# Performance work log

Hardware: AMD Instinct MI355X
Metric: run time of the kernel (lower is better)

Reference implementation:

```python
import jax, jax.numpy as jnp
import numpy as np

NUM_HEADS = 12
DIM = 768
HEAD_DIM = DIM // NUM_HEADS
SCALE = HEAD_DIM ** -0.5
LORA_ALPHA = 1.0


def setup_inputs() -> dict:
    key = jax.random.key(0)
    ks = jax.random.split(key, 9)
    B, H, W = 1, 64, 64
    return {
        "x": jax.random.normal(ks[0], (B, H, W, DIM), jnp.float32),
        "w_qkv": jax.random.normal(ks[1], (3 * DIM, DIM), jnp.float32) * 0.02,
        "b_qkv": jax.random.normal(ks[2], (3 * DIM,), jnp.float32) * 0.02,
        "lora_A": jax.random.normal(ks[3], (12, DIM), jnp.float32) * 0.02,
        "lora_B": jax.random.normal(ks[4], (3 * DIM, 12), jnp.float32) * 0.02,
        "w_proj": jax.random.normal(ks[5], (DIM, DIM), jnp.float32) * 0.02,
        "b_proj": jax.random.normal(ks[6], (DIM,), jnp.float32) * 0.02,
        "rel_pos_h": jax.random.normal(ks[7], (2 * H - 1, HEAD_DIM), jnp.float32) * 0.02,
        "rel_pos_w": jax.random.normal(ks[8], (2 * W - 1, HEAD_DIM), jnp.float32) * 0.02,
    }


def _get_rel_pos(size: int, rel_pos: jnp.ndarray) -> jnp.ndarray:
    # q_size == k_size and rel_pos.shape[0] == 2*size-1, so no interpolation.
    coords = jnp.arange(size)[:, None] - jnp.arange(size)[None, :] + (size - 1)
    return rel_pos[coords]  # [size, size, head_dim]


def reference(x, w_qkv, b_qkv, lora_A, lora_B, w_proj, b_proj, rel_pos_h, rel_pos_w):
    B, H, W, _ = x.shape
    N = H * W
    # LoRA qkv projection: W_eff path = base + alpha * x @ (B A)^T
    qkv = x @ w_qkv.T + b_qkv + LORA_ALPHA * ((x @ lora_A.T) @ lora_B.T)
    qkv = qkv.reshape(B, N, 3, NUM_HEADS, HEAD_DIM)
    qkv = jnp.transpose(qkv, (2, 0, 3, 1, 4)).reshape(3, B * NUM_HEADS, N, HEAD_DIM)
    q, k, v = qkv[0], qkv[1], qkv[2]
    attn = jnp.einsum('bqc,bkc->bqk', q * SCALE, k)  # [B*nh, N, N]
    # decomposed relative position bias
    Rh = _get_rel_pos(H, rel_pos_h)  # [H, H, hd]
    Rw = _get_rel_pos(W, rel_pos_w)  # [W, W, hd]
    r_q = q.reshape(B * NUM_HEADS, H, W, HEAD_DIM)
    rel_h = jnp.einsum('bhwc,hkc->bhwk', r_q, Rh)
    rel_w = jnp.einsum('bhwc,wkc->bhwk', r_q, Rw)
    attn = (attn.reshape(-1, H, W, H, W)
            + rel_h[:, :, :, :, None]
            + rel_w[:, :, :, None, :]).reshape(-1, N, N)
    attn = jax.nn.softmax(attn, axis=-1)
    out = jnp.einsum('bqk,bkc->bqc', attn, v)  # [B*nh, N, hd]
    out = out.reshape(B, NUM_HEADS, H, W, HEAD_DIM)
    out = jnp.transpose(out, (0, 2, 3, 1, 4)).reshape(B, H, W, DIM)
    return out @ w_proj.T + b_proj
```

## Files before the change

### kernel.cpp

```cpp
#include <hip/hip_runtime.h>
#include <stdint.h>


typedef __attribute__((ext_vector_type(4))) float f32x4;
typedef __attribute__((ext_vector_type(16))) float f32x16;
typedef __attribute__((ext_vector_type(4))) float fvec4;
typedef __attribute__((ext_vector_type(8))) short s16x8;
typedef __attribute__((ext_vector_type(4))) short s16x4;
typedef __attribute__((ext_vector_type(4))) unsigned u32x4;

constexpr int NH  = 12;
constexpr int HD  = 64;
constexpr int DIM = 768;
constexpr int N   = 4096;
constexpr int QKV = 2304;
constexpr float LOG2E  = 1.4426950408889634f;
constexpr float SCALE2 = 0.125f * LOG2E;

static __device__ __forceinline__ short f2bf(float f) {
  unsigned u = __builtin_bit_cast(unsigned, f);
  unsigned r = (u + 0x7FFFu + ((u >> 16) & 1u)) >> 16;
  return (short)r;
}
static __device__ __forceinline__ float bf2f(short s) {
  unsigned u = ((unsigned)(unsigned short)s) << 16;
  return __builtin_bit_cast(float, u);
}
static __device__ __forceinline__ unsigned cvt_pk_bf16(float a, float b) {
  unsigned r;
  asm("v_cvt_pk_bf16_f32 %0, %1, %2" : "=v"(r) : "v"(a), "v"(b));
  return r;
}
static __device__ __forceinline__ float ex2(float x) {
  float r;
  asm("v_exp_f32 %0, %1" : "=v"(r) : "v"(x));
  return r;
}
static __device__ __forceinline__ void gload16(const void* g, void* l) {
  __builtin_amdgcn_global_load_lds(
      (const __attribute__((address_space(1))) void*)g,
      (__attribute__((address_space(3))) void*)l, 16, 0, 0);
}

__global__ __launch_bounds__(256) void k_weff(const float* __restrict__ w_qkv,
                                              const float* __restrict__ lora_A,
                                              const float* __restrict__ lora_B,
                                              short* __restrict__ weff) {
  int e = blockIdx.x * 256 + threadIdx.x;
  if (e >= QKV * DIM) return;
  int r = e / DIM, c = e % DIM;
  float acc = w_qkv[e];
#pragma unroll
  for (int t = 0; t < 12; ++t) acc += lora_B[r * 12 + t] * lora_A[t * DIM + c];
  weff[e] = f2bf(acc);
}

__global__ __launch_bounds__(256) void k_x2bf(const float* __restrict__ x,
                                              short* __restrict__ xb) {
  int i = blockIdx.x * 256 + threadIdx.x;
  fvec4 v = *reinterpret_cast<const fvec4*>(x + (size_t)i * 4);
  s16x4 p;
  p[0] = f2bf(v[0]); p[1] = f2bf(v[1]); p[2] = f2bf(v[2]); p[3] = f2bf(v[3]);
  *reinterpret_cast<s16x4*>(xb + (size_t)i * 4) = p;
}

__global__ __launch_bounds__(256) void k_wsplit(const float* __restrict__ w,
                                                short* __restrict__ ws) {
  int r = blockIdx.y;
  int kk = blockIdx.x * 256 + threadIdx.x;
  int blk = (kk >= 1536) ? 2 : (kk >= 768 ? 1 : 0);
  int c = kk - blk * 768;
  float wv = w[(size_t)r * 768 + c];
  short hi = f2bf(wv);
  ws[(size_t)r * 2304 + kk] = (blk == 1) ? f2bf(wv - bf2f(hi)) : hi;
}

template <int KIT, int MODE, int BM>
__global__ __launch_bounds__(256) void k_gemm(const short* __restrict__ A,
                                              const short* __restrict__ B,
                                              const float* __restrict__ bias,
                                              short* __restrict__ qo,
                                              short* __restrict__ ko,
                                              short* __restrict__ vo,
                                              float* __restrict__ outf) {
  constexpr int MFR = BM / 32;
  __shared__ __align__(16) char lds[BM * 128 + 16384];
  const int tid = threadIdx.x;
  const int wave = tid >> 6, lane = tid & 63, lr = lane & 15, lg = lane >> 4;
  const int wr = wave >> 1, wc = wave & 1;
  const int i0 = blockIdx.x * BM, j0 = blockIdx.y * 128;
  const int LDA = KIT * 128;

  size_t offA[MFR], offB[4];
#pragma unroll
  for (int it = 0; it < MFR; ++it) {
    int c = it * 256 + tid;
    int row = c >> 3;
    offA[it] = (size_t)row * LDA + (((c & 7) << 4) ^ ((row & 7) << 4));
  }
#pragma unroll
  for (int it = 0; it < 4; ++it) {
    int c = it * 256 + tid;
    int row = c >> 3;
    offB[it] = (size_t)row * LDA + (((c & 7) << 4) ^ ((row & 7) << 4));
  }
  const char* Ab = (const char*)A + (size_t)i0 * LDA;
  const char* Bb = (const char*)B + (size_t)j0 * LDA;
  char* la = lds + wave * 1024;
  char* lb = lds + BM * 128 + wave * 1024;

  const int swz = (lr & 7) << 4;
  const int ab = (wr * (BM / 2) + lr) * 128 + ((lg * 16) ^ swz);
  const int bb = BM * 128 + (wc * 64 + lr) * 128 + ((lg * 16) ^ swz);

  f32x4 acc[MFR][4] = {};

  for (int kt = 0; kt < KIT; ++kt) {
    const size_t kadd = (size_t)kt * 128;
#pragma unroll
    for (int it = 0; it < MFR; ++it) gload16(Ab + kadd + offA[it], la + it * 4096);
#pragma unroll
    for (int it = 0; it < 4; ++it) gload16(Bb + kadd + offB[it], lb + it * 4096);
    __syncthreads();
#pragma unroll
    for (int ks2 = 0; ks2 < 2; ++ks2) {
      s16x8 af[MFR], bf_[4];
#pragma unroll
      for (int m = 0; m < MFR; ++m)
        af[m] = *reinterpret_cast<const s16x8*>(lds + ((ab + m * 2048) ^ (ks2 << 6)));
#pragma unroll
      for (int n = 0; n < 4; ++n)
        bf_[n] = *reinterpret_cast<const s16x8*>(lds + ((bb + n * 2048) ^ (ks2 << 6)));
#pragma unroll
      for (int m = 0; m < MFR; ++m)
#pragma unroll
        for (int n = 0; n < 4; ++n)
          acc[m][n] = __builtin_amdgcn_mfma_f32_16x16x32_bf16(af[m], bf_[n], acc[m][n], 0, 0, 0);
    }
    __syncthreads();
  }

  if constexpr (MODE == 0) {
    const int three = j0 / 768;
    const int head = ((j0 % 768) >> 6) + wc;
    short* dst = (three == 0) ? qo : ((three == 1) ? ko : vo);
#pragma unroll
    for (int n = 0; n < 4; ++n) {
      const int col = n * 16 + lr;
      const float bj = bias[j0 + wc * 64 + col];
#pragma unroll
      for (int m = 0; m < MFR; ++m)
#pragma unroll
        for (int r = 0; r < 4; ++r) {
          int i = i0 + wr * (BM / 2) + m * 16 + lg * 4 + r;
          dst[((size_t)head * N + i) * HD + col] = f2bf(acc[m][n][r] + bj);
        }
    }
  } else {
#pragma unroll
    for (int n = 0; n < 4; ++n) {
      const int j = j0 + wc * 64 + n * 16 + lr;
      const float bj = bias[j];
#pragma unroll
      for (int m = 0; m < MFR; ++m)
#pragma unroll
        for (int r = 0; r < 4; ++r) {
          int i = i0 + wr * (BM / 2) + m * 16 + lg * 4 + r;
          outf[(size_t)i * 768 + j] = acc[m][n][r] + bj;
        }
    }
  }
}

__global__ __launch_bounds__(256) void k_vT(const short* __restrict__ vg,
                                            short* __restrict__ vTg) {
  __shared__ short ts[64 * 72];
  const int tid = threadIdx.x;
  const int i0 = blockIdx.x * 64;
  const int h = blockIdx.y;
#pragma unroll
  for (int it = 0; it < 2; ++it) {
    int ch = tid + 256 * it;
    int row = ch >> 3, cc = (ch & 7) * 8;
    *reinterpret_cast<s16x8*>(&ts[row * 72 + cc]) =
        *reinterpret_cast<const s16x8*>(&vg[((size_t)h * N + i0 + row) * HD + cc]);
  }
  __syncthreads();
#pragma unroll
  for (int it = 0; it < 2; ++it) {
    int ch = tid + 256 * it;
    int c = ch >> 3, ii = (ch & 7) * 8;
    s16x8 o;
#pragma unroll
    for (int j = 0; j < 8; ++j) o[j] = ts[(ii + j) * 72 + c];
    *reinterpret_cast<s16x8*>(&vTg[((size_t)h * HD + c) * N + i0 + ii]) = o;
  }
}

__global__ __launch_bounds__(256) void k_relh(const short* __restrict__ qg,
                                              const float* __restrict__ tab,
                                              short* __restrict__ rhT) {
  __shared__ short Ts[64 * 72];
  const int tid = threadIdx.x;
  const int wave = tid >> 6, lane = tid & 63, lr = lane & 15, lg = lane >> 4;
  const int h = blockIdx.x >> 6, qh = blockIdx.x & 63;
#pragma unroll
  for (int it = 0; it < 4; ++it) {
    int e = tid + 256 * it;
    int row = e >> 4, c4 = (e & 15) * 4;
    fvec4 v = *reinterpret_cast<const fvec4*>(tab + (size_t)(qh + 63 - row) * 64 + c4);
    s16x4 p;
    p[0] = f2bf(v[0]); p[1] = f2bf(v[1]); p[2] = f2bf(v[2]); p[3] = f2bf(v[3]);
    *reinterpret_cast<s16x4*>(&Ts[row * 72 + c4]) = p;
  }
  __syncthreads();
  const size_t qrow = (size_t)h * N + qh * 64 + wave * 16 + lr;
  const s16x8 a0 = *reinterpret_cast<const s16x8*>(qg + qrow * 64 + lg * 8);
  const s16x8 a1 = *reinterpret_cast<const s16x8*>(qg + qrow * 64 + 32 + lg * 8);
  f32x4 acc[4] = {};
#pragma unroll
  for (int ks2 = 0; ks2 < 2; ++ks2)
#pragma unroll
    for (int n = 0; n < 4; ++n) {
      s16x8 b = *reinterpret_cast<const s16x8*>(&Ts[(n * 16 + lr) * 72 + ks2 * 32 + lg * 8]);
      acc[n] = __builtin_amdgcn_mfma_f32_16x16x32_bf16(ks2 ? a1 : a0, b, acc[n], 0, 0, 0);
    }
  const size_t ob = ((size_t)(h * 64 + qh)) * 4096;
#pragma unroll
  for (int n = 0; n < 4; ++n) {
    s16x4 o;
#pragma unroll
    for (int r = 0; r < 4; ++r) o[r] = f2bf(acc[n][r]);
    *reinterpret_cast<s16x4*>(&rhT[ob + (size_t)(n * 16 + lr) * 64 + wave * 16 + lg * 4]) = o;
  }
}

__global__ __launch_bounds__(256) void k_relw(const short* __restrict__ qg,
                                              const float* __restrict__ tab,
                                              short* __restrict__ rwg) {
  __shared__ short Ts[128 * 72];
  const int tid = threadIdx.x;
  const int wave = tid >> 6, lane = tid & 63, lr = lane & 15, lg = lane >> 4;
  const int h = blockIdx.x >> 6, qh = blockIdx.x & 63;
#pragma unroll
  for (int it = 0; it < 8; ++it) {
    int e = tid + 256 * it;
    int row = e >> 4, c4 = (e & 15) * 4;
    s16x4 p = {0, 0, 0, 0};
    if (row < 127) {
      fvec4 v = *reinterpret_cast<const fvec4*>(tab + (size_t)row * 64 + c4);
      p[0] = f2bf(v[0]); p[1] = f2bf(v[1]); p[2] = f2bf(v[2]); p[3] = f2bf(v[3]);
    }
    *reinterpret_cast<s16x4*>(&Ts[row * 72 + c4]) = p;
  }
  __syncthreads();
  const size_t qrow = (size_t)h * N + qh * 64 + wave * 16 + lr;
  const s16x8 a0 = *reinterpret_cast<const s16x8*>(qg + qrow * 64 + lg * 8);
  const s16x8 a1 = *reinterpret_cast<const s16x8*>(qg + qrow * 64 + 32 + lg * 8);
  f32x4 acc[8] = {};
#pragma unroll
  for (int ks2 = 0; ks2 < 2; ++ks2)
#pragma unroll
    for (int n = 0; n < 8; ++n) {
      s16x8 b = *reinterpret_cast<const s16x8*>(&Ts[(n * 16 + lr) * 72 + ks2 * 32 + lg * 8]);
      acc[n] = __builtin_amdgcn_mfma_f32_16x16x32_bf16(ks2 ? a1 : a0, b, acc[n], 0, 0, 0);
    }
  const size_t ob = ((size_t)h * N + qh * 64) * 64;
#pragma unroll
  for (int n = 0; n < 8; ++n) {
    int d = n * 16 + lr;
#pragma unroll
    for (int r = 0; r < 4; ++r) {
      int qw = wave * 16 + lg * 4 + r;
      int kw = qw + 63 - d;
      if ((unsigned)kw < 64u) rwg[ob + (size_t)qw * 64 + kw] = f2bf(acc[n][r]);
    }
  }
}

#define QG_BLOCK(QB0, QB1, QB2, QB3, RW, RH2, ACC0, ACC1, LA, LB)              \
  do {                                                                         \
    f32x16 sa = {};                                                            \
    __builtin_amdgcn_s_setprio(1);                                             \
    sa = __builtin_amdgcn_mfma_f32_32x32x16_bf16(kf0, QB0, sa, 0, 0, 0);       \
    sa = __builtin_amdgcn_mfma_f32_32x32x16_bf16(kf1, QB1, sa, 0, 0, 0);       \
    sa = __builtin_amdgcn_mfma_f32_32x32x16_bf16(kf2, QB2, sa, 0, 0, 0);       \
    sa = __builtin_amdgcn_mfma_f32_32x32x16_bf16(kf3, QB3, sa, 0, 0, 0);       \
    __builtin_amdgcn_s_setprio(0);                                             \
    float p[16];                                                               \
    _Pragma("unroll")                                                          \
    for (int reg = 0; reg < 16; ++reg)                                         \
      p[reg] = ex2(fmaf(sa[reg], SCALE2, RH2 + RW[reg]));                      \
    float t0 = (p[0] + p[1]) + (p[2] + p[3]);                                  \
    float t1 = (p[4] + p[5]) + (p[6] + p[7]);                                  \
    float t2 = (p[8] + p[9]) + (p[10] + p[11]);                                \
    float t3 = (p[12] + p[13]) + (p[14] + p[15]);                              \
    LA += t0 + t1;                                                             \
    LB += t2 + t3;                                                             \
    unsigned w00 = cvt_pk_bf16(p[0], p[1]),   w01 = cvt_pk_bf16(p[2], p[3]);   \
    unsigned w10 = cvt_pk_bf16(p[4], p[5]),   w11 = cvt_pk_bf16(p[6], p[7]);   \
    unsigned w20 = cvt_pk_bf16(p[8], p[9]),   w21 = cvt_pk_bf16(p[10], p[11]); \
    unsigned w30 = cvt_pk_bf16(p[12], p[13]), w31 = cvt_pk_bf16(p[14], p[15]); \
    asm("v_permlane32_swap_b32 %0, %1" : "+v"(w00), "+v"(w10));                \
    asm("v_permlane32_swap_b32 %0, %1" : "+v"(w01), "+v"(w11));                \
    asm("v_permlane32_swap_b32 %0, %1" : "+v"(w20), "+v"(w30));                \
    asm("v_permlane32_swap_b32 %0, %1" : "+v"(w21), "+v"(w31));                \
    u32x4 u0 = {w00, w01, w10, w11};                                           \
    u32x4 u1 = {w20, w21, w30, w31};                                           \
    s16x8 pa0 = __builtin_bit_cast(s16x8, u0);                                 \
    s16x8 pa1 = __builtin_bit_cast(s16x8, u1);                                 \
    __builtin_amdgcn_s_setprio(1);                                             \
    ACC0 = __builtin_amdgcn_mfma_f32_32x32x16_bf16(pa0, vf0, ACC0, 0, 0, 0);   \
    ACC0 = __builtin_amdgcn_mfma_f32_32x32x16_bf16(pa1, vf2, ACC0, 0, 0, 0);   \
    ACC1 = __builtin_amdgcn_mfma_f32_32x32x16_bf16(pa0, vf1, ACC1, 0, 0, 0);   \
    ACC1 = __builtin_amdgcn_mfma_f32_32x32x16_bf16(pa1, vf3, ACC1, 0, 0, 0);   \
    __builtin_amdgcn_s_setprio(0);                                             \
  } while (0)

__global__ __launch_bounds__(256, 2) void k_flash(const short* __restrict__ qg,
                                                  const short* __restrict__ kg,
                                                  const short* __restrict__ vTg,
                                                  const short* __restrict__ rhTg,
                                                  const short* __restrict__ rwg,
                                                  short* __restrict__ aprime) {
  __shared__ __align__(16) char lds[65536];
  const int tid = threadIdx.x;
  const int wave = tid >> 6, lane = tid & 63;
  const int ql = lane & 31, hi = lane >> 5;
  const int kt2 = wave & 1, kh2 = wave >> 1;
  const int bid = blockIdx.x;
  const int id = (bid & 7) * 96 + (bid >> 3);
  const int h = id >> 6, qt = id & 63;
  const int i0 = qt * 64;

  const short* q0p = qg + ((size_t)h * N + i0 + ql) * 64 + hi * 8;
  const short* q1p = q0p + 32 * 64;
  const s16x8 qb00 = *reinterpret_cast<const s16x8*>(q0p);
  const s16x8 qb01 = *reinterpret_cast<const s16x8*>(q0p + 16);
  const s16x8 qb02 = *reinterpret_cast<const s16x8*>(q0p + 32);
  const s16x8 qb03 = *reinterpret_cast<const s16x8*>(q0p + 48);
  const s16x8 qb10 = *reinterpret_cast<const s16x8*>(q1p);
  const s16x8 qb11 = *reinterpret_cast<const s16x8*>(q1p + 16);
  const s16x8 qb12 = *reinterpret_cast<const s16x8*>(q1p + 32);
  const s16x8 qb13 = *reinterpret_cast<const s16x8*>(q1p + 48);

  f32x16 rw0, rw1;
  {
    const short* rwp0 = rwg + ((size_t)h * N + i0 + ql) * 64 + kh2 * 32 + hi * 4;
    const short* rwp1 = rwp0 + 32 * 64;
#pragma unroll
    for (int reg = 0; reg < 16; ++reg) {
      int o = (reg & 3) + 8 * (reg >> 2);
      rw0[reg] = LOG2E * bf2f(rwp0[o]);
      rw1[reg] = LOG2E * bf2f(rwp1[o]);
    }
  }
  const short* rhp = rhTg + ((size_t)(h * 64 + qt)) * 4096;

  int soff[8];
  const char* sbase;
  if (wave < 2) {
    sbase = (const char*)kg + (size_t)h * N * 128 + wave * 64 * 128;
#pragma unroll
    for (int it = 0; it < 8; ++it) {
      int c = it * 64 + lane, row = c >> 3;
      soff[it] = row * 128 + (((c & 7) << 4) ^ ((row & 7) << 4));
    }
  } else {
    sbase = (const char*)vTg + (size_t)h * 64 * 8192 + (wave - 2) * 128;
#pragma unroll
    for (int it = 0; it < 8; ++it) {
      int c = it * 64 + lane, r = c >> 3;
      soff[it] = r * 8192 + (((c & 7) << 4) ^ ((r & 7) << 4));
    }
  }
  const int sstep = (wave < 2) ? 16384 : 256;
  char* lreg = lds + wave * 8192;

  auto STAGE = [&](int i, int buf) {
    const char* sp = sbase + (size_t)i * sstep;
    char* lp = lreg + buf * 32768;
#pragma unroll
    for (int it = 0; it < 8; ++it) gload16(sp + soff[it], lp + it * 1024);
  };

  const int swzq = (ql & 7) << 4;
  const int krow = (kt2 * 64 + kh2 * 32 + ql) * 128;
  const int kco0 = krow + ((0 * 32 + hi * 16) ^ swzq);
  const int kco1 = krow + ((1 * 32 + hi * 16) ^ swzq);
  const int kco2 = krow + ((2 * 32 + hi * 16) ^ swzq);
  const int kco3 = krow + ((3 * 32 + hi * 16) ^ swzq);
  const int vrow0 = 16384 + kt2 * 8192 + ql * 128;
  const int vrow1 = vrow0 + 32 * 128;
  const int vch0 = (kh2 * 64 + 0 * 32 + hi * 16) ^ swzq;
  const int vch1 = (kh2 * 64 + 1 * 32 + hi * 16) ^ swzq;
  const int vco0 = vrow0 + vch0;
  const int vco1 = vrow1 + vch0;
  const int vco2 = vrow0 + vch1;
  const int vco3 = vrow1 + vch1;

  f32x16 acc00 = {}, acc01 = {}, acc10 = {}, acc11 = {};
  float la0 = 0.f, lb0 = 0.f, la1 = 0.f, lb1 = 0.f;

  unsigned short rhc0 = (unsigned short)rhp[(size_t)kt2 * 64 + ql];
  unsigned short rhc1 = (unsigned short)rhp[(size_t)kt2 * 64 + 32 + ql];

  STAGE(0, 0);
  __syncthreads();

  for (int i = 0; i < 32; ++i) {
    const int buf = i & 1;
    if (i + 1 < 32) STAGE(i + 1, buf ^ 1);
    const int nx = (i + 1 < 32) ? i + 1 : 31;
    unsigned short rhn0 = (unsigned short)rhp[(size_t)(nx * 2 + kt2) * 64 + ql];
    unsigned short rhn1 = (unsigned short)rhp[(size_t)(nx * 2 + kt2) * 64 + 32 + ql];

    const char* bufp = lds + buf * 32768;
    s16x8 kf0 = *reinterpret_cast<const s16x8*>(bufp + kco0);
    s16x8 kf1 = *reinterpret_cast<const s16x8*>(bufp + kco1);
    s16x8 kf2 = *reinterpret_cast<const s16x8*>(bufp + kco2);
    s16x8 kf3 = *reinterpret_cast<const s16x8*>(bufp + kco3);
    s16x8 vf0 = *reinterpret_cast<const s16x8*>(bufp + vco0);
    s16x8 vf1 = *reinterpret_cast<const s16x8*>(bufp + vco1);
    s16x8 vf2 = *reinterpret_cast<const s16x8*>(bufp + vco2);
    s16x8 vf3 = *reinterpret_cast<const s16x8*>(bufp + vco3);

    const float rh20 = LOG2E * bf2f((short)rhc0);
    const float rh21 = LOG2E * bf2f((short)rhc1);

    QG_BLOCK(qb00, qb01, qb02, qb03, rw0, rh20, acc00, acc01, la0, lb0);
    QG_BLOCK(qb10, qb11, qb12, qb13, rw1, rh21, acc10, acc11, la1, lb1);

    rhc0 = rhn0; rhc1 = rhn1;
    __syncthreads();
  }

  float l0 = la0 + lb0, l1 = la1 + lb1;
  l0 += __shfl_xor(l0, 32);
  l1 += __shfl_xor(l1, 32);
  float* LS = (float*)lds;
  if (lane < 32) {
    LS[wave * 64 + ql] = l0;
    LS[wave * 64 + 32 + ql] = l1;
  }
  __syncthreads();
  const int eq = wave * 16 + (lane >> 2);
  const int cb = (lane & 3) * 16;
  float inv = 1.0f / (LS[eq] + LS[64 + eq] + LS[128 + eq] + LS[192 + eq]);
  __syncthreads();
  float* OF = (float*)lds;
#pragma unroll
  for (int qg2 = 0; qg2 < 2; ++qg2)
#pragma unroll
    for (int ct = 0; ct < 2; ++ct) {
      const f32x16& a = qg2 ? (ct ? acc11 : acc10) : (ct ? acc01 : acc00);
#pragma unroll
      for (int reg = 0; reg < 16; ++reg) {
        int q = qg2 * 32 + (reg & 3) + 8 * (reg >> 2) + 4 * hi;
        int c = ct * 32 + ql;
        OF[wave * 4096 + q * 64 + (c ^ ((q & 7) << 2))] = a[reg];
      }
    }
  __syncthreads();
  f32x4 osum[4] = {};
#pragma unroll
  for (int w = 0; w < 4; ++w)
#pragma unroll
    for (int j = 0; j < 4; ++j)
      osum[j] += *reinterpret_cast<const f32x4*>(
          &OF[w * 4096 + eq * 64 + ((cb + j * 4) ^ ((eq & 7) << 2))]);

  s16x8 hi8[2], lo8[2];
#pragma unroll
  for (int j = 0; j < 4; ++j)
#pragma unroll
    for (int e = 0; e < 4; ++e) {
      float o = osum[j][e] * inv;
      short oh = f2bf(o);
      float lo = o - bf2f(oh);
      int idx = j * 4 + e;
      hi8[idx >> 3][idx & 7] = oh;
      lo8[idx >> 3][idx & 7] = f2bf(lo);
    }
  size_t obase = (size_t)(i0 + eq) * 2304 + h * 64 + cb;
  *reinterpret_cast<s16x8*>(&aprime[obase]) = hi8[0];
  *reinterpret_cast<s16x8*>(&aprime[obase + 8]) = hi8[1];
  *reinterpret_cast<s16x8*>(&aprime[obase + 768]) = hi8[0];
  *reinterpret_cast<s16x8*>(&aprime[obase + 776]) = hi8[1];
  *reinterpret_cast<s16x8*>(&aprime[obase + 1536]) = lo8[0];
  *reinterpret_cast<s16x8*>(&aprime[obase + 1544]) = lo8[1];
}

extern "C" void kernel_launch(void* const* d_in, const int* in_sizes, int n_in,
                              void* d_out, int out_size, void* d_ws, size_t ws_size,
                              hipStream_t stream) {
  const float* x      = (const float*)d_in[0];
  const float* w_qkv  = (const float*)d_in[1];
  const float* b_qkv  = (const float*)d_in[2];
  const float* lora_A = (const float*)d_in[3];
  const float* lora_B = (const float*)d_in[4];
  const float* w_proj = (const float*)d_in[5];
  const float* b_proj = (const float*)d_in[6];
  const float* rel_h  = (const float*)d_in[7];
  const float* rel_w  = (const float*)d_in[8];
  float* out = (float*)d_out;

  char* ws = (char*)d_ws;
  short* weff   = (short*)(ws + 0);
  short* xb     = (short*)(ws + 3538944);
  short* vg     = (short*)(ws + 9830400);
  short* aprime = (short*)(ws + 0);
  short* qg     = (short*)(ws + 18874368);
  short* kg     = (short*)(ws + 25165824);
  short* vTg    = (short*)(ws + 31457280);
  short* rhT    = (short*)(ws + 37748736);
  short* rwg    = (short*)(ws + 44040192);
  short* wsp    = (short*)(ws + 50331648);
  (void)ws_size; (void)in_sizes; (void)n_in; (void)out_size;

  k_weff<<<dim3((QKV * DIM + 255) / 256), dim3(256), 0, stream>>>(w_qkv, lora_A, lora_B, weff);
  k_x2bf<<<dim3(3072), dim3(256), 0, stream>>>(x, xb);
  k_wsplit<<<dim3(9, 768), dim3(256), 0, stream>>>(w_proj, wsp);
  k_gemm<12, 0, 128><<<dim3(32, 18), dim3(256), 0, stream>>>(xb, weff, b_qkv, qg, kg, vg, nullptr);
  k_vT<<<dim3(64, NH), dim3(256), 0, stream>>>(vg, vTg);
  k_relh<<<dim3(NH * 64), dim3(256), 0, stream>>>(qg, rel_h, rhT);
  k_relw<<<dim3(NH * 64), dim3(256), 0, stream>>>(qg, rel_w, rwg);
  k_flash<<<dim3(NH * 64), dim3(256), 0, stream>>>(qg, kg, vTg, rhT, rwg, aprime);
  k_gemm<36, 1, 64><<<dim3(64, 6), dim3(256), 0, stream>>>(aprime, wsp, b_proj, nullptr, nullptr, nullptr, out);
}
```

Before: 179.8 us.

## Double-buffer GEMM LDS tiles and use partial vmcnt waits in flash loop

The GEMM kernel gains a second LDS buffer so the next K tile is prefetched with global_load_lds while the current one is consumed. Explicit partial s_waitcnt vmcnt waits plus raw s_barrier and sched_barrier replace __syncthreads, so the newest prefetches can stay in flight. The flash attention loop is unrolled by two with fixed buffer offsets and uses the same partial-wait barrier scheme instead of the full drain implied by __syncthreads. This doubles GEMM LDS use and adds occupancy 2 launch bounds. The hand-counted vmcnt values must match the issued loads exactly or results will be corrupted.

New measurement: 171.2 us. 4.8% less time.

```diff
diff --git a/kernel.cpp b/kernel.cpp
--- a/kernel.cpp
+++ b/kernel.cpp
@@ -40,6 +40,15 @@
   __builtin_amdgcn_global_load_lds(
       (const __attribute__((address_space(1))) void*)g,
       (__attribute__((address_space(3))) void*)l, 16, 0, 0);
+}
+static __device__ __forceinline__ void barrier_pre() {
+  __builtin_amdgcn_s_barrier();
+  __builtin_amdgcn_sched_barrier(0);
+}
+static __device__ __forceinline__ void barrier_post() {
+  __builtin_amdgcn_sched_barrier(0);
+  __builtin_amdgcn_s_barrier();
+  __builtin_amdgcn_sched_barrier(0);
 }
 
 __global__ __launch_bounds__(256) void k_weff(const float* __restrict__ w_qkv,
@@ -76,15 +85,16 @@
 }
 
 template <int KIT, int MODE, int BM>
-__global__ __launch_bounds__(256) void k_gemm(const short* __restrict__ A,
-                                              const short* __restrict__ B,
-                                              const float* __restrict__ bias,
-                                              short* __restrict__ qo,
-                                              short* __restrict__ ko,
-                                              short* __restrict__ vo,
-                                              float* __restrict__ outf) {
+__global__ __launch_bounds__(256, 2) void k_gemm(const short* __restrict__ A,
+                                                 const short* __restrict__ B,
+                                                 const float* __restrict__ bias,
+                                                 short* __restrict__ qo,
+                                                 short* __restrict__ ko,
+                                                 short* __restrict__ vo,
+                                                 float* __restrict__ outf) {
   constexpr int MFR = BM / 32;
-  __shared__ __align__(16) char lds[BM * 128 + 16384];
+  constexpr int BUFB = BM * 128 + 16384;
+  __shared__ __align__(16) char lds[2 * BUFB];
   const int tid = threadIdx.x;
   const int wave = tid >> 6, lane = tid & 63, lr = lane & 15, lg = lane >> 4;
   const int wr = wave >> 1, wc = wave & 1;
@@ -106,8 +116,17 @@
   }
   const char* Ab = (const char*)A + (size_t)i0 * LDA;
   const char* Bb = (const char*)B + (size_t)j0 * LDA;
-  char* la = lds + wave * 1024;
-  char* lb = lds + BM * 128 + wave * 1024;
+
+  auto STAGE = [&](int kt, int b) {
+    char* base = lds + b * BUFB;
+    const size_t kadd = (size_t)kt * 128;
+#pragma unroll
+    for (int it = 0; it < MFR; ++it)
+      gload16(Ab + kadd + offA[it], base + wave * 1024 + it * 4096);
+#pragma unroll
+    for (int it = 0; it < 4; ++it)
+      gload16(Bb + kadd + offB[it], base + BM * 128 + wave * 1024 + it * 4096);
+  };
 
   const int swz = (lr & 7) << 4;
   const int ab = (wr * (BM / 2) + lr) * 128 + ((lg * 16) ^ swz);
@@ -115,29 +134,36 @@
 
   f32x4 acc[MFR][4] = {};
 
+  STAGE(0, 0);
   for (int kt = 0; kt < KIT; ++kt) {
-    const size_t kadd = (size_t)kt * 128;
-#pragma unroll
-    for (int it = 0; it < MFR; ++it) gload16(Ab + kadd + offA[it], la + it * 4096);
-#pragma unroll
-    for (int it = 0; it < 4; ++it) gload16(Bb + kadd + offB[it], lb + it * 4096);
-    __syncthreads();
+    const int buf = kt & 1;
+    if (kt + 1 < KIT) {
+      STAGE(kt + 1, buf ^ 1);
+      if constexpr (BM == 128)
+        asm volatile("s_waitcnt vmcnt(8)" ::: "memory");
+      else
+        asm volatile("s_waitcnt vmcnt(6)" ::: "memory");
+    } else {
+      asm volatile("s_waitcnt vmcnt(0)" ::: "memory");
+    }
+    barrier_pre();
+    const char* bufp = lds + buf * BUFB;
 #pragma unroll
     for (int ks2 = 0; ks2 < 2; ++ks2) {
       s16x8 af[MFR], bf_[4];
 #pragma unroll
       for (int m = 0; m < MFR; ++m)
-        af[m] = *reinterpret_cast<const s16x8*>(lds + ((ab + m * 2048) ^ (ks2 << 6)));
+        af[m] = *reinterpret_cast<const s16x8*>(bufp + ((ab + m * 2048) ^ (ks2 << 6)));
 #pragma unroll
       for (int n = 0; n < 4; ++n)
-        bf_[n] = *reinterpret_cast<const s16x8*>(lds + ((bb + n * 2048) ^ (ks2 << 6)));
+        bf_[n] = *reinterpret_cast<const s16x8*>(bufp + ((bb + n * 2048) ^ (ks2 << 6)));
 #pragma unroll
       for (int m = 0; m < MFR; ++m)
 #pragma unroll
         for (int n = 0; n < 4; ++n)
           acc[m][n] = __builtin_amdgcn_mfma_f32_16x16x32_bf16(af[m], bf_[n], acc[m][n], 0, 0, 0);
     }
-    __syncthreads();
+    barrier_post();
   }
 
   if constexpr (MODE == 0) {
@@ -317,6 +343,23 @@
     __builtin_amdgcn_s_setprio(0);                                             \
   } while (0)
 
+#define FLASH_BODY(BUFOFF, RHU0, RHU1)                                         \
+  do {                                                                         \
+    const char* bufp = lds + (BUFOFF);                                         \
+    s16x8 kf0 = *reinterpret_cast<const s16x8*>(bufp + kco0);                  \
+    s16x8 kf1 = *reinterpret_cast<const s16x8*>(bufp + kco1);                  \
+    s16x8 kf2 = *reinterpret_cast<const s16x8*>(bufp + kco2);                  \
+    s16x8 kf3 = *reinterpret_cast<const s16x8*>(bufp + kco3);                  \
+    s16x8 vf0 = *reinterpret_cast<const s16x8*>(bufp + vco0);                  \
+    s16x8 vf1 = *reinterpret_cast<const s16x8*>(bufp + vco1);                  \
+    s16x8 vf2 = *reinterpret_cast<const s16x8*>(bufp + vco2);                  \
+    s16x8 vf3 = *reinterpret_cast<const s16x8*>(bufp + vco3);                  \
+    const float rh20 = LOG2E * bf2f((short)(RHU0));                            \
+    const float rh21 = LOG2E * bf2f((short)(RHU1));                            \
+    QG_BLOCK(qb00, qb01, qb02, qb03, rw0, rh20, acc00, acc01, la0, lb0);       \
+    QG_BLOCK(qb10, qb11, qb12, qb13, rw1, rh21, acc10, acc11, la1, lb1);       \
+  } while (0)
+
 __global__ __launch_bounds__(256, 2) void k_flash(const short* __restrict__ qg,
                                                   const short* __restrict__ kg,
                                                   const short* __restrict__ vTg,
@@ -402,37 +445,31 @@
   f32x16 acc00 = {}, acc01 = {}, acc10 = {}, acc11 = {};
   float la0 = 0.f, lb0 = 0.f, la1 = 0.f, lb1 = 0.f;
 
-  unsigned short rhc0 = (unsigned short)rhp[(size_t)kt2 * 64 + ql];
-  unsigned short rhc1 = (unsigned short)rhp[(size_t)kt2 * 64 + 32 + ql];
-
   STAGE(0, 0);
-  __syncthreads();
-
-  for (int i = 0; i < 32; ++i) {
-    const int buf = i & 1;
-    if (i + 1 < 32) STAGE(i + 1, buf ^ 1);
-    const int nx = (i + 1 < 32) ? i + 1 : 31;
-    unsigned short rhn0 = (unsigned short)rhp[(size_t)(nx * 2 + kt2) * 64 + ql];
-    unsigned short rhn1 = (unsigned short)rhp[(size_t)(nx * 2 + kt2) * 64 + 32 + ql];
-
-    const char* bufp = lds + buf * 32768;
-    s16x8 kf0 = *reinterpret_cast<const s16x8*>(bufp + kco0);
-    s16x8 kf1 = *reinterpret_cast<const s16x8*>(bufp + kco1);
-    s16x8 kf2 = *reinterpret_cast<const s16x8*>(bufp + kco2);
-    s16x8 kf3 = *reinterpret_cast<const s16x8*>(bufp + kco3);
-    s16x8 vf0 = *reinterpret_cast<const s16x8*>(bufp + vco0);
-    s16x8 vf1 = *reinterpret_cast<const s16x8*>(bufp + vco1);
-    s16x8 vf2 = *reinterpret_cast<const s16x8*>(bufp + vco2);
-    s16x8 vf3 = *reinterpret_cast<const s16x8*>(bufp + vco3);
-
-    const float rh20 = LOG2E * bf2f((short)rhc0);
-    const float rh21 = LOG2E * bf2f((short)rhc1);
-
-    QG_BLOCK(qb00, qb01, qb02, qb03, rw0, rh20, acc00, acc01, la0, lb0);
-    QG_BLOCK(qb10, qb11, qb12, qb13, rw1, rh21, acc10, acc11, la1, lb1);
-
-    rhc0 = rhn0; rhc1 = rhn1;
-    __syncthreads();
+  unsigned short rA0 = (unsigned short)rhp[(size_t)kt2 * 64 + ql];
+  unsigned short rA1 = (unsigned short)rhp[(size_t)kt2 * 64 + 32 + ql];
+  unsigned short rB0 = 0, rB1 = 0;
+
+  for (int ii = 0; ii < 16; ++ii) {
+    const int i = 2 * ii;
+    STAGE(i + 1, 1);
+    rB0 = (unsigned short)rhp[(size_t)((i + 1) * 2 + kt2) * 64 + ql];
+    rB1 = (unsigned short)rhp[(size_t)((i + 1) * 2 + kt2) * 64 + 32 + ql];
+    asm volatile("s_waitcnt vmcnt(10)" ::: "memory");
+    barrier_pre();
+    FLASH_BODY(0, rA0, rA1);
+    barrier_post();
+    if (i + 2 < 32) {
+      STAGE(i + 2, 0);
+      rA0 = (unsigned short)rhp[(size_t)((i + 2) * 2 + kt2) * 64 + ql];
+      rA1 = (unsigned short)rhp[(size_t)((i + 2) * 2 + kt2) * 64 + 32 + ql];
+      asm volatile("s_waitcnt vmcnt(10)" ::: "memory");
+    } else {
+      asm volatile("s_waitcnt vmcnt(0)" ::: "memory");
+    }
+    barrier_pre();
+    FLASH_BODY(32768, rB0, rB1);
+    barrier_post();
   }
 
   float l0 = la0 + lb0, l1 = la1 + lb1;
```

## Double-buffer GEMM LDS tiles and fold softmax scales into producers

Applied to the files above, without the earlier changes.

The projection GEMM now double-buffers its LDS tiles. It issues global-to-LDS loads for the next k-step before computing the current one and waits with explicit vmcnt counts and split barriers, so load latency overlaps MFMA work. It also moves the softmax scale and LOG2E factors upstream into the K projection epilogue and the rel-pos kernels, which removes per-element multiplies from the attention inner loop. In exchange, LDS use doubles, which may limit occupancy, and the hand-set vmcnt values must match the number of loads per stage. K and the bias terms are also rounded to bf16 after scaling, which slightly changes precision.

Measured after the change: 161.0 us. 1.12x faster.

```diff
diff --git a/kernel.cpp b/kernel.cpp
--- a/kernel.cpp
+++ b/kernel.cpp
@@ -40,6 +40,15 @@
   __builtin_amdgcn_global_load_lds(
       (const __attribute__((address_space(1))) void*)g,
       (__attribute__((address_space(3))) void*)l, 16, 0, 0);
+}
+static __device__ __forceinline__ void barrier_pre() {
+  __builtin_amdgcn_s_barrier();
+  __builtin_amdgcn_sched_barrier(0);
+}
+static __device__ __forceinline__ void barrier_post() {
+  __builtin_amdgcn_sched_barrier(0);
+  __builtin_amdgcn_s_barrier();
+  __builtin_amdgcn_sched_barrier(0);
 }
 
 __global__ __launch_bounds__(256) void k_weff(const float* __restrict__ w_qkv,
@@ -76,15 +85,16 @@
 }
 
 template <int KIT, int MODE, int BM>
-__global__ __launch_bounds__(256) void k_gemm(const short* __restrict__ A,
-                                              const short* __restrict__ B,
-                                              const float* __restrict__ bias,
-                                              short* __restrict__ qo,
-                                              short* __restrict__ ko,
-                                              short* __restrict__ vo,
-                                              float* __restrict__ outf) {
+__global__ __launch_bounds__(256, 2) void k_gemm(const short* __restrict__ A,
+                                                 const short* __restrict__ B,
+                                                 const float* __restrict__ bias,
+                                                 short* __restrict__ qo,
+                                                 short* __restrict__ ko,
+                                                 short* __restrict__ vo,
+                                                 float* __restrict__ outf) {
   constexpr int MFR = BM / 32;
-  __shared__ __align__(16) char lds[BM * 128 + 16384];
+  constexpr int BUFB = BM * 128 + 16384;
+  __shared__ __align__(16) char lds[2 * BUFB];
   const int tid = threadIdx.x;
   const int wave = tid >> 6, lane = tid & 63, lr = lane & 15, lg = lane >> 4;
   const int wr = wave >> 1, wc = wave & 1;
@@ -106,8 +116,17 @@
   }
   const char* Ab = (const char*)A + (size_t)i0 * LDA;
   const char* Bb = (const char*)B + (size_t)j0 * LDA;
-  char* la = lds + wave * 1024;
-  char* lb = lds + BM * 128 + wave * 1024;
+
+  auto STAGE = [&](int kt, int b) {
+    char* base = lds + b * BUFB;
+    const size_t kadd = (size_t)kt * 128;
+#pragma unroll
+    for (int it = 0; it < MFR; ++it)
+      gload16(Ab + kadd + offA[it], base + wave * 1024 + it * 4096);
+#pragma unroll
+    for (int it = 0; it < 4; ++it)
+      gload16(Bb + kadd + offB[it], base + BM * 128 + wave * 1024 + it * 4096);
+  };
 
   const int swz = (lr & 7) << 4;
   const int ab = (wr * (BM / 2) + lr) * 128 + ((lg * 16) ^ swz);
@@ -115,34 +134,42 @@
 
   f32x4 acc[MFR][4] = {};
 
+  STAGE(0, 0);
   for (int kt = 0; kt < KIT; ++kt) {
-    const size_t kadd = (size_t)kt * 128;
-#pragma unroll
-    for (int it = 0; it < MFR; ++it) gload16(Ab + kadd + offA[it], la + it * 4096);
-#pragma unroll
-    for (int it = 0; it < 4; ++it) gload16(Bb + kadd + offB[it], lb + it * 4096);
-    __syncthreads();
+    const int buf = kt & 1;
+    if (kt + 1 < KIT) {
+      STAGE(kt + 1, buf ^ 1);
+      if constexpr (BM == 128)
+        asm volatile("s_waitcnt vmcnt(8)" ::: "memory");
+      else
+        asm volatile("s_waitcnt vmcnt(6)" ::: "memory");
+    } else {
+      asm volatile("s_waitcnt vmcnt(0)" ::: "memory");
+    }
+    barrier_pre();
+    const char* bufp = lds + buf * BUFB;
 #pragma unroll
     for (int ks2 = 0; ks2 < 2; ++ks2) {
       s16x8 af[MFR], bf_[4];
 #pragma unroll
       for (int m = 0; m < MFR; ++m)
-        af[m] = *reinterpret_cast<const s16x8*>(lds + ((ab + m * 2048) ^ (ks2 << 6)));
+        af[m] = *reinterpret_cast<const s16x8*>(bufp + ((ab + m * 2048) ^ (ks2 << 6)));
 #pragma unroll
       for (int n = 0; n < 4; ++n)
-        bf_[n] = *reinterpret_cast<const s16x8*>(lds + ((bb + n * 2048) ^ (ks2 << 6)));
+        bf_[n] = *reinterpret_cast<const s16x8*>(bufp + ((bb + n * 2048) ^ (ks2 << 6)));
 #pragma unroll
       for (int m = 0; m < MFR; ++m)
 #pragma unroll
         for (int n = 0; n < 4; ++n)
           acc[m][n] = __builtin_amdgcn_mfma_f32_16x16x32_bf16(af[m], bf_[n], acc[m][n], 0, 0, 0);
     }
-    __syncthreads();
+    barrier_post();
   }
 
   if constexpr (MODE == 0) {
     const int three = j0 / 768;
     const int head = ((j0 % 768) >> 6) + wc;
+    const float osc = (three == 1) ? SCALE2 : 1.0f;
     short* dst = (three == 0) ? qo : ((three == 1) ? ko : vo);
 #pragma unroll
     for (int n = 0; n < 4; ++n) {
@@ -153,7 +180,7 @@
 #pragma unroll
         for (int r = 0; r < 4; ++r) {
           int i = i0 + wr * (BM / 2) + m * 16 + lg * 4 + r;
-          dst[((size_t)head * N + i) * HD + col] = f2bf(acc[m][n][r] + bj);
+          dst[((size_t)head * N + i) * HD + col] = f2bf((acc[m][n][r] + bj) * osc);
         }
     }
   } else {
@@ -230,7 +257,7 @@
   for (int n = 0; n < 4; ++n) {
     s16x4 o;
 #pragma unroll
-    for (int r = 0; r < 4; ++r) o[r] = f2bf(acc[n][r]);
+    for (int r = 0; r < 4; ++r) o[r] = f2bf(acc[n][r] * LOG2E);
     *reinterpret_cast<s16x4*>(&rhT[ob + (size_t)(n * 16 + lr) * 64 + wave * 16 + lg * 4]) = o;
   }
 }
@@ -273,7 +300,7 @@
     for (int r = 0; r < 4; ++r) {
       int qw = wave * 16 + lg * 4 + r;
       int kw = qw + 63 - d;
-      if ((unsigned)kw < 64u) rwg[ob + (size_t)qw * 64 + kw] = f2bf(acc[n][r]);
+      if ((unsigned)kw < 64u) rwg[ob + (size_t)qw * 64 + kw] = f2bf(acc[n][r] * LOG2E);
     }
   }
 }
@@ -290,7 +317,7 @@
     float p[16];                                                               \
     _Pragma("unroll")                                                          \
     for (int reg = 0; reg < 16; ++reg)                                         \
-      p[reg] = ex2(fmaf(sa[reg], SCALE2, RH2 + RW[reg]));                      \
+      p[reg] = ex2(sa[reg] + RH2 + RW[reg]);                                   \
     float t0 = (p[0] + p[1]) + (p[2] + p[3]);                                  \
     float t1 = (p[4] + p[5]) + (p[6] + p[7]);                                  \
     float t2 = (p[8] + p[9]) + (p[10] + p[11]);                                \
@@ -351,8 +378,8 @@
 #pragma unroll
     for (int reg = 0; reg < 16; ++reg) {
       int o = (reg & 3) + 8 * (reg >> 2);
-      rw0[reg] = LOG2E * bf2f(rwp0[o]);
-      rw1[reg] = LOG2E * bf2f(rwp1[o]);
+      rw0[reg] = bf2f(rwp0[o]);
+      rw1[reg] = bf2f(rwp1[o]);
     }
   }
   const short* rhp = rhTg + ((size_t)(h * 64 + qt)) * 4096;
@@ -425,8 +452,8 @@
     s16x8 vf2 = *reinterpret_cast<const s16x8*>(bufp + vco2);
     s16x8 vf3 = *reinterpret_cast<const s16x8*>(bufp + vco3);
 
-    const float rh20 = LOG2E * bf2f((short)rhc0);
-    const float rh21 = LOG2E * bf2f((short)rhc1);
+    const float rh20 = bf2f((short)rhc0);
+    const float rh21 = bf2f((short)rhc1);
 
     QG_BLOCK(qb00, qb01, qb02, qb03, rw0, rh20, acc00, acc01, la0, lb0);
     QG_BLOCK(qb10, qb11, qb12, qb13, rw1, rh21, acc10, acc11, la1, lb1);
```
